# Optimization experiments

Hardware: AMD Instinct MI355X
Metric: run time of the kernel (lower is better)

Reference implementation:

```python
import jax, jax.numpy as jnp
import numpy as np

N_NODES = 50000
N_EDGES = 800000
IN_F, EDGE_F, HID, HEADS, OUT_F = 128, 16, 32, 4, 128
NEG_SLOPE = 0.2


def edge_gat_layer(h, ef, src, dst, W, We, al, ar, ae, b, act):
    """One DGL-style EdgeGATConv layer.
    h: [N, Fin], ef: [E, Fe], W: [Fin, H*D], We: [Fe, H*D],
    al/ar/ae: [H, D], b: [H*D]. Returns [N, H*D].
    """
    N = h.shape[0]
    H, D = al.shape
    feat = (h @ W).reshape(N, H, D)                    # [N,H,D]
    fe = (ef @ We).reshape(-1, H, D)                   # [E,H,D]
    el = jnp.einsum('nhd,hd->nh', feat, al)            # [N,H]
    er = jnp.einsum('nhd,hd->nh', feat, ar)            # [N,H]
    ee = jnp.einsum('ehd,hd->eh', fe, ae)              # [E,H]
    e = jax.nn.leaky_relu(el[src] + er[dst] + ee, NEG_SLOPE)  # [E,H]
    # edge softmax over incoming edges of each dst node
    emax = jax.ops.segment_max(e, dst, num_segments=N)        # [N,H]
    ex = jnp.exp(e - emax[dst])                               # [E,H]
    esum = jax.ops.segment_sum(ex, dst, num_segments=N)       # [N,H]
    a = ex / esum[dst]                                        # [E,H]
    msg = feat[src] * a[:, :, None]                           # [E,H,D]
    rst = jax.ops.segment_sum(msg, dst, num_segments=N)       # [N,H,D]
    rst = rst + b.reshape(1, H, D)
    if act:
        rst = jax.nn.relu(rst)
    return rst.reshape(N, H * D)


def _glorot(k, shape):
    fan = shape[0]
    return jax.random.normal(k, shape, dtype=jnp.float32) / np.sqrt(fan)


def setup_inputs() -> dict:
    key = jax.random.key(0)
    ks = jax.random.split(key, 24)
    inp = {
        'h': jax.random.normal(ks[0], (N_NODES, IN_F), dtype=jnp.float32),
        'edge_feats': jax.random.normal(ks[1], (N_EDGES, EDGE_F), dtype=jnp.float32),
        'src': jax.random.randint(ks[2], (N_EDGES,), 0, N_NODES, dtype=jnp.int32),
        'dst': jax.random.randint(ks[3], (N_EDGES,), 0, N_NODES, dtype=jnp.int32),
    }
    # layer 0: IN_F -> HEADS*HID ; layer 1: HEADS*HID -> HEADS*HID ; layer 2: heads=1, OUT_F
    dims = [(IN_F, HEADS, HID), (HEADS * HID, HEADS, HID), (HEADS * HID, 1, OUT_F)]
    ki = 4
    for i, (fin, H, D) in enumerate(dims):
        inp[f'W{i}'] = _glorot(ks[ki], (fin, H * D)); ki += 1
        inp[f'We{i}'] = _glorot(ks[ki], (EDGE_F, H * D)); ki += 1
        inp[f'al{i}'] = _glorot(ks[ki], (H, D)); ki += 1
        inp[f'ar{i}'] = _glorot(ks[ki], (H, D)); ki += 1
        inp[f'ae{i}'] = _glorot(ks[ki], (H, D)); ki += 1
        inp[f'b{i}'] = jnp.zeros((H * D,), dtype=jnp.float32)
    return inp


def reference(h, edge_feats, src, dst,
              W0, We0, al0, ar0, ae0, b0,
              W1, We1, al1, ar1, ae1, b1,
              W2, We2, al2, ar2, ae2, b2):
    h = edge_gat_layer(h, edge_feats, src, dst, W0, We0, al0, ar0, ae0, b0, True)
    h = edge_gat_layer(h, edge_feats, src, dst, W1, We1, al1, ar1, ae1, b1, True)
    h = edge_gat_layer(h, edge_feats, src, dst, W2, We2, al2, ar2, ae2, b2, False)
    return h
```

## Files before the change

### kernel.cpp

```cpp
#include <hip/hip_runtime.h>
#include <hip/hip_fp16.h>
#include <cstdint>

#define NN 50000
#define NE 800000
static constexpr int HD = 128;
static constexpr int EF_DIM = 16;
static constexpr int SCAN_B = 256;
static constexpr int NPARTS = (NN + SCAN_B - 1) / SCAN_B;
static constexpr int EBLK = (NE + 255) / 256;
static constexpr int FG = (NN + 63) / 64;

typedef _Float16 f16x4 __attribute__((ext_vector_type(4)));
typedef float f32x4 __attribute__((ext_vector_type(4)));

struct RecP {
    int src;
    int e;
    f16x4 p0;
    f16x4 p1;
    _Float16 p2;
    _Float16 pad;
};
union Rec32 { RecP r; float4 v[2]; };


__global__ void k_zero(int* __restrict__ cnt) {
    int i = blockIdx.x * blockDim.x + threadIdx.x;
    if (i < NN) cnt[i] = 0;
}

__global__ __launch_bounds__(256) void k_prep2(const float* __restrict__ h,
        const int* __restrict__ dst,
        const float* __restrict__ We0, const float* __restrict__ ae0,
        const float* __restrict__ We1, const float* __restrict__ ae1,
        const float* __restrict__ We2, const float* __restrict__ ae2,
        const float* __restrict__ W0, const float* __restrict__ W1,
        const float* __restrict__ W2,
        int* __restrict__ cnt, int* __restrict__ pos_loc, float* __restrict__ M,
        _Float16* __restrict__ Wht, _Float16* __restrict__ Xh) {
    int b = blockIdx.x;
    const int t = threadIdx.x;
    if (b < EBLK) {
        int e = b * 256 + t;
        if (e < NE) pos_loc[e] = atomicAdd(&cnt[dst[e]], 1);
        return;
    }
    b -= EBLK;
    if (b < 3) {
        int l = b;
        const float* We = (l == 0) ? We0 : (l == 1) ? We1 : We2;
        const float* ae = (l == 0) ? ae0 : (l == 1) ? ae1 : ae2;
        int H = (l == 2) ? 1 : 4, D = (l == 2) ? 128 : 32;
        if (t < EF_DIM * H) {
            int f = t / H, hh = t % H;
            float s = 0.f;
            for (int d = 0; d < D; d++) s += We[f * HD + hh * D + d] * ae[hh * D + d];
            M[l * 64 + f * H + hh] = s;
        }
        return;
    }
    if (b < 195) {
        int i = (b - 3) * 256 + t;
        int l = i >> 14, rem = i & 16383;
        int n = rem >> 7, k = rem & 127;
        const float* W = (l == 0) ? W0 : (l == 1) ? W1 : W2;
        Wht[(size_t)l * 16384 + n * 128 + k] = (_Float16)W[k * 128 + n];
        return;
    }
    {
        int i = (b - 195) * 256 + t;
        if (i < NN * 32) {
            float4 v = ((const float4*)h)[i];
            f16x4 o = {(_Float16)v.x, (_Float16)v.y, (_Float16)v.z, (_Float16)v.w};
            ((f16x4*)Xh)[i] = o;
        }
    }
}

__global__ __launch_bounds__(SCAN_B) void k_part(const int* __restrict__ deg,
                                                 int* __restrict__ part) {
    __shared__ int s[SCAN_B];
    int t = threadIdx.x;
    int i = blockIdx.x * SCAN_B + t;
    s[t] = (i < NN) ? deg[i] : 0;
    __syncthreads();
    for (int off = SCAN_B / 2; off > 0; off >>= 1) {
        if (t < off) s[t] += s[t + off];
        __syncthreads();
    }
    if (t == 0) part[blockIdx.x] = s[0];
}

__global__ __launch_bounds__(SCAN_B) void k_scanpart(int* __restrict__ part) {
    __shared__ int s[SCAN_B];
    int t = threadIdx.x;
    int v = (t < NPARTS) ? part[t] : 0;
    s[t] = v;
    __syncthreads();
    for (int off = 1; off < SCAN_B; off <<= 1) {
        int u = (t >= off) ? s[t - off] : 0;
        __syncthreads();
        s[t] += u;
        __syncthreads();
    }
    if (t < NPARTS) part[t] = s[t] - v;
}

__global__ __launch_bounds__(SCAN_B) void k_rowptr(const int* __restrict__ deg,
                                                   const int* __restrict__ part,
                                                   int* __restrict__ row_ptr) {
    __shared__ int s[SCAN_B];
    int t = threadIdx.x;
    int i = blockIdx.x * SCAN_B + t;
    int v = (i < NN) ? deg[i] : 0;
    s[t] = v;
    __syncthreads();
    for (int off = 1; off < SCAN_B; off <<= 1) {
        int u = (t >= off) ? s[t - off] : 0;
        __syncthreads();
        s[t] += u;
        __syncthreads();
    }
    int excl = s[t] - v + part[blockIdx.x];
    if (i < NN) row_ptr[i] = excl;
    if (i == NN) row_ptr[NN] = NE;
}

__global__ __launch_bounds__(256) void k_place(const int* __restrict__ src,
                                               const int* __restrict__ dst,
                                               const int* __restrict__ pos_loc,
                                               const float* __restrict__ EFt,
                                               const float* __restrict__ M,
                                               const int* __restrict__ row_ptr,
                                               float4* __restrict__ rec) {
    __shared__ float sM[192];
    int t = threadIdx.x;
    if (t < 192) sM[t] = M[t];
    __syncthreads();
    int e = blockIdx.x * 256 + t;
    if (e >= NE) return;
    float ef[EF_DIM];
    const float4* efp = (const float4*)(EFt + (size_t)e * EF_DIM);
#pragma unroll
    for (int q = 0; q < 4; q++) {
        float4 v = efp[q];
        ef[4 * q] = v.x; ef[4 * q + 1] = v.y; ef[4 * q + 2] = v.z; ef[4 * q + 3] = v.w;
    }
    float o0[4] = {0.f, 0.f, 0.f, 0.f};
    float o1[4] = {0.f, 0.f, 0.f, 0.f};
    float o2 = 0.f;
#pragma unroll
    for (int f = 0; f < EF_DIM; f++) {
        float v = ef[f];
#pragma unroll
        for (int hh = 0; hh < 4; hh++) {
            o0[hh] += v * sM[f * 4 + hh];
            o1[hh] += v * sM[64 + f * 4 + hh];
        }
        o2 += v * sM[128 + f];
    }
    Rec32 u;
    u.r.src = src[e];
    u.r.e = e;
    u.r.p0 = f16x4{(_Float16)o0[0], (_Float16)o0[1], (_Float16)o0[2], (_Float16)o0[3]};
    u.r.p1 = f16x4{(_Float16)o1[0], (_Float16)o1[1], (_Float16)o1[2], (_Float16)o1[3]};
    u.r.p2 = (_Float16)o2;
    u.r.pad = (_Float16)0.f;
    int pos = row_ptr[dst[e]] + pos_loc[e];
    rec[(size_t)pos * 2] = u.v[0];
    rec[(size_t)pos * 2 + 1] = u.v[1];
}

__global__ __launch_bounds__(256) void k_segsort2(const int* __restrict__ row_ptr,
                                                  const float4* __restrict__ rec,
                                                  int* __restrict__ ssrc,
                                                  f16x4* __restrict__ ep0,
                                                  f16x4* __restrict__ ep1,
                                                  _Float16* __restrict__ ep2) {
    __shared__ Rec32 seg[4][128];
    const int wave = threadIdx.x >> 6;
    const int lane = threadIdx.x & 63;
    const int n = blockIdx.x * 4 + wave;
    const int start = row_ptr[n];
    const int len = row_ptr[n + 1] - start;
    const bool small = (len > 0 && len <= 128);
    if (small)
        for (int s = lane; s < len; s += 64) {
            seg[wave][s].v[0] = rec[(size_t)(start + s) * 2];
            seg[wave][s].v[1] = rec[(size_t)(start + s) * 2 + 1];
        }
    __syncthreads();
    if (small) {
        for (int s = lane; s < len; s += 64) {
            RecP me = seg[wave][s].r;
            int rank = 0;
            for (int j = 0; j < len; j++) {
                const RecP& o = seg[wave][j].r;
                rank += (o.src < me.src) || (o.src == me.src && o.e < me.e);
            }
            int w = start + rank;
            ssrc[w] = me.src;
            ep0[w] = me.p0;
            ep1[w] = me.p1;
            ep2[w] = me.p2;
        }
    } else if (len > 128) {
        for (int s = lane; s < len; s += 64) {
            Rec32 u;
            u.v[0] = rec[(size_t)(start + s) * 2];
            u.v[1] = rec[(size_t)(start + s) * 2 + 1];
            int w = start + s;
            ssrc[w] = u.r.src;
            ep0[w] = u.r.p0;
            ep1[w] = u.r.p1;
            ep2[w] = u.r.p2;
        }
    }
}

template <int H>
__global__ __launch_bounds__(256) void k_feat(const _Float16* __restrict__ Xh,
                                              const _Float16* __restrict__ Wht,
                                              const float* __restrict__ al,
                                              const float* __restrict__ ar,
                                              _Float16* __restrict__ Fh,
                                              float* __restrict__ el,
                                              float* __restrict__ er) {
    const int t = threadIdx.x;
    const int lane = t & 63;
    const int wv = t >> 6;
    const int l15 = lane & 15;
    const int kg = lane >> 4;
    const int nbase = blockIdx.x * 64;
    const int arow = nbase + wv * 16 + l15;
    const int rclamp = (arow < NN) ? arow : NN - 1;
    const int ksub = kg * 4;
    f16x4 a[8];
#pragma unroll
    for (int kb = 0; kb < 8; kb++)
        a[kb] = *(const f16x4*)(Xh + (size_t)rclamp * 128 + kb * 16 + ksub);

    const int r0 = nbase + wv * 16 + kg * 4;
    float slp[4][H], srp[4][H];
#pragma unroll
    for (int r = 0; r < 4; r++)
#pragma unroll
        for (int hh = 0; hh < H; hh++) { slp[r][hh] = 0.f; srp[r][hh] = 0.f; }

#pragma unroll
    for (int nt = 0; nt < 8; nt++) {
        f32x4 acc = {0.f, 0.f, 0.f, 0.f};
        const int nc = nt * 16 + l15;
        const _Float16* wp = Wht + (size_t)nc * 128;
#pragma unroll
        for (int kb = 0; kb < 8; kb++) {
            f16x4 bf = *(const f16x4*)(wp + kb * 16 + ksub);
            acc = __builtin_amdgcn_mfma_f32_16x16x16f16(a[kb], bf, acc, 0, 0, 0);
        }
        const float alv = al[nc], arv = ar[nc];
        const int hsel = (H == 4) ? (nt >> 1) : 0;
#pragma unroll
        for (int r = 0; r < 4; r++) {
            int ro = r0 + r;
            if (ro < NN) Fh[(size_t)ro * 128 + nc] = (_Float16)acc[r];
            slp[r][hsel] += acc[r] * alv;
            srp[r][hsel] += acc[r] * arv;
        }
    }

#pragma unroll
    for (int m = 1; m < 16; m <<= 1)
#pragma unroll
        for (int r = 0; r < 4; r++)
#pragma unroll
            for (int hh = 0; hh < H; hh++) {
                slp[r][hh] += __shfl_xor(slp[r][hh], m);
                srp[r][hh] += __shfl_xor(srp[r][hh], m);
            }

    if (H == 4) {
        int r = l15 >> 2, hh2 = l15 & 3;
        float sv = 0.f, ev = 0.f;
#pragma unroll
        for (int rr = 0; rr < 4; rr++)
#pragma unroll
            for (int hc = 0; hc < H; hc++)
                if (rr == r && hc == hh2) { sv = slp[rr][hc]; ev = srp[rr][hc]; }
        int ro = r0 + r;
        if (ro < NN) { el[ro * 4 + hh2] = sv; er[ro * 4 + hh2] = ev; }
    } else {
        if (l15 < 4) {
            float sv = 0.f, ev = 0.f;
#pragma unroll
            for (int rr = 0; rr < 4; rr++)
                if (rr == l15) { sv = slp[rr][0]; ev = srp[rr][0]; }
            int ro = r0 + l15;
            if (ro < NN) { el[ro] = sv; er[ro] = ev; }
        }
    }
}

template <int H, int D, int OUT16>
__global__ __launch_bounds__(256) void k_node(const int* __restrict__ row_ptr,
                                              const int* __restrict__ ssrc,
                                              const _Float16* __restrict__ ep,
                                              const float* __restrict__ el,
                                              const float* __restrict__ er,
                                              const __half2* __restrict__ Fh,
                                              const float* __restrict__ bias,
                                              float* __restrict__ Rf,
                                              _Float16* __restrict__ Rh,
                                              int act) {
    __shared__ float wlds[4][256];
    const int wave = threadIdx.x >> 6;
    const int lane = threadIdx.x & 63;
    const int n = blockIdx.x * 4 + wave;
    const int start = row_ptr[n];
    const int end = row_ptr[n + 1];
    const int len = end - start;
    const int slots = len * H;
    const int c = 2 * lane;
    const int hcol = c / D;
    float2 b2 = make_float2(bias[c], bias[c + 1]);
    float2 a = make_float2(0.f, 0.f);

    if (len > 0) {
        constexpr int hsh = (H == 4) ? 2 : 0;
        const int hh = lane & (H - 1);
        const float er_j = er[n * H + hh];
        const _Float16* epb = ep + (size_t)start * H;
        float pmax = -3.0e38f, psum = 0.f;

        if (slots <= 256) {
            float* wp = wlds[wave];
            for (int jj = lane; jj < slots; jj += 64) {
                int i = start + (jj >> hsh);
                float x = el[ssrc[i] * H + hh] + er_j + (float)epb[jj];
                x = (x > 0.f) ? x : 0.2f * x;
                wp[jj] = x;
                pmax = fmaxf(pmax, x);
            }
            for (int m = H; m < 64; m <<= 1) pmax = fmaxf(pmax, __shfl_xor(pmax, m));
            for (int jj = lane; jj < slots; jj += 64) {
                float ex = __expf(wp[jj] - pmax);
                wp[jj] = ex;
                psum += ex;
            }
            for (int m = H; m < 64; m <<= 1) psum += __shfl_xor(psum, m);
            const float inv = 1.f / __shfl(psum, hcol);
#pragma unroll 8
            for (int i = start; i < end; i++) {
                float w = wp[(i - start) * H + hcol];
                float2 f2 = __half22float2(Fh[(size_t)ssrc[i] * 64 + lane]);
                a.x += f2.x * w;
                a.y += f2.y * w;
            }
            a.x *= inv;
            a.y *= inv;
        } else {
            for (int jj = lane; jj < slots; jj += 64) {
                int i = start + (jj >> hsh);
                float x = el[ssrc[i] * H + hh] + er_j + (float)epb[jj];
                x = (x > 0.f) ? x : 0.2f * x;
                pmax = fmaxf(pmax, x);
            }
            for (int m = H; m < 64; m <<= 1) pmax = fmaxf(pmax, __shfl_xor(pmax, m));
            for (int jj = lane; jj < slots; jj += 64) {
                int i = start + (jj >> hsh);
                float x = el[ssrc[i] * H + hh] + er_j + (float)epb[jj];
                x = (x > 0.f) ? x : 0.2f * x;
                psum += __expf(x - pmax);
            }
            for (int m = H; m < 64; m <<= 1) psum += __shfl_xor(psum, m);
            const float inv = 1.f / __shfl(psum, hcol);
            const float pm_c = __shfl(pmax, hcol);
            const float er_c = er[n * H + hcol];
            for (int i = start; i < end; i++) {
                int sn = ssrc[i];
                float x = el[sn * H + hcol] + er_c + (float)epb[(i - start) * H + hcol];
                x = (x > 0.f) ? x : 0.2f * x;
                float w = __expf(x - pm_c);
                float2 f2 = __half22float2(Fh[(size_t)sn * 64 + lane]);
                a.x += f2.x * w;
                a.y += f2.y * w;
            }
            a.x *= inv;
            a.y *= inv;
        }
    }

    float2 v = make_float2(a.x + b2.x, a.y + b2.y);
    if (act) { v.x = fmaxf(v.x, 0.f); v.y = fmaxf(v.y, 0.f); }
    if (OUT16)
        ((__half2*)Rh)[(size_t)n * 64 + lane] = __floats2half2_rn(v.x, v.y);
    else
        ((float2*)Rf)[(size_t)n * 64 + lane] = v;
}


extern "C" void kernel_launch(void* const* d_in, const int* in_sizes, int n_in,
                              void* d_out, int out_size, void* d_ws, size_t ws_size,
                              hipStream_t stream) {
    const float* h   = (const float*)d_in[0];
    const float* eft = (const float*)d_in[1];
    const int* src   = (const int*)d_in[2];
    const int* dst   = (const int*)d_in[3];
    auto P = [&](int i) { return (const float*)d_in[i]; };

    float* ws = (float*)d_ws;
    float4* rec    = (float4*)ws;
    _Float16* Xh   = (_Float16*)(ws + 6400000);
    _Float16* Wht  = Xh + (size_t)NN * 128;
    _Float16* ep0s = Wht + 3 * 16384;
    _Float16* ep1s = ep0s + (size_t)NE * 4;
    _Float16* ep2s = ep1s + (size_t)NE * 4;
    int* ssrc      = (int*)(ep2s + NE);
    int* pos_loc   = ssrc + NE;
    float* M       = (float*)(pos_loc + NE);
    int* row_ptr   = (int*)(M + 192);
    int* cnt       = row_ptr + (NN + 1);
    int* part      = cnt + NN;
    _Float16* Fh   = (_Float16*)(part + NPARTS + 64);
    float* el      = (float*)(Fh + (size_t)NN * 128);
    float* er      = el + (size_t)NN * 4;
    float* out     = (float*)d_out;

    hipLaunchKernelGGL(k_zero, dim3(NPARTS), dim3(256), 0, stream, cnt);
    hipLaunchKernelGGL(k_prep2, dim3(EBLK + 195 + (NN * 32 + 255) / 256), dim3(256), 0,
                       stream, h, dst, P(5), P(8), P(11), P(14), P(17), P(20),
                       P(4), P(10), P(16), cnt, pos_loc, M, Wht, Xh);
    hipLaunchKernelGGL(k_part, dim3(NPARTS), dim3(SCAN_B), 0, stream, cnt, part);
    hipLaunchKernelGGL(k_scanpart, dim3(1), dim3(SCAN_B), 0, stream, part);
    hipLaunchKernelGGL(k_rowptr, dim3(NPARTS), dim3(SCAN_B), 0, stream,
                       cnt, part, row_ptr);
    hipLaunchKernelGGL(k_place, dim3(EBLK), dim3(256), 0, stream,
                       src, dst, pos_loc, eft, M, row_ptr, rec);
    hipLaunchKernelGGL((k_feat<4>), dim3(FG), dim3(256), 0, stream,
                       Xh, Wht, P(6), P(7), Fh, el, er);
    hipLaunchKernelGGL(k_segsort2, dim3(NN / 4), dim3(256), 0, stream,
                       row_ptr, rec, ssrc, (f16x4*)ep0s, (f16x4*)ep1s, ep2s);

    hipLaunchKernelGGL((k_node<4, 32, 1>), dim3(NN / 4), dim3(256), 0, stream,
                       row_ptr, ssrc, ep0s, el, er, (const __half2*)Fh, P(9),
                       nullptr, Xh, 1);
    hipLaunchKernelGGL((k_feat<4>), dim3(FG), dim3(256), 0, stream,
                       Xh, Wht + 16384, P(12), P(13), Fh, el, er);
    hipLaunchKernelGGL((k_node<4, 32, 1>), dim3(NN / 4), dim3(256), 0, stream,
                       row_ptr, ssrc, ep1s, el, er, (const __half2*)Fh, P(15),
                       nullptr, Xh, 1);
    hipLaunchKernelGGL((k_feat<1>), dim3(FG), dim3(256), 0, stream,
                       Xh, Wht + 32768, P(18), P(19), Fh, el, er);
    hipLaunchKernelGGL((k_node<1, 128, 0>), dim3(NN / 4), dim3(256), 0, stream,
                       row_ptr, ssrc, ep2s, el, er, (const __half2*)Fh, P(21),
                       out, nullptr, 0);
}
```

Measured before the change: 370.6 us.

## Replace three-kernel row-pointer scan with single-pass decoupled look-back scan

Merges the partial-sum, partition-scan and row-pointer kernels into one kernel that uses decoupled look-back over per-block flag/value state words, which k_zero now clears. The aim is to drop two kernel launches and the extra passes over the degree array. It also moves k_segsort2 ahead of the first k_feat and lowers the unroll factor in the node aggregation loop from 8 to 4. Look-back relies on earlier blocks being scheduled before later ones finish spinning, which is normally true but is not formally guaranteed.

```diff
diff --git a/kernel.cpp b/kernel.cpp
--- a/kernel.cpp
+++ b/kernel.cpp
@@ -25,9 +25,10 @@
 union Rec32 { RecP r; float4 v[2]; };
 
 
-__global__ void k_zero(int* __restrict__ cnt) {
+__global__ void k_zero(int* __restrict__ cnt, unsigned* __restrict__ state) {
     int i = blockIdx.x * blockDim.x + threadIdx.x;
     if (i < NN) cnt[i] = 0;
+    if (i < NPARTS) state[i] = 0;
 }
 
 __global__ __launch_bounds__(256) void k_prep2(const float* __restrict__ h,
@@ -78,24 +79,14 @@
     }
 }
 
-__global__ __launch_bounds__(SCAN_B) void k_part(const int* __restrict__ deg,
-                                                 int* __restrict__ part) {
+__global__ __launch_bounds__(SCAN_B) void k_scan_lb(const int* __restrict__ cnt,
+                                                    int* __restrict__ row_ptr,
+                                                    unsigned* __restrict__ state) {
     __shared__ int s[SCAN_B];
-    int t = threadIdx.x;
-    int i = blockIdx.x * SCAN_B + t;
-    s[t] = (i < NN) ? deg[i] : 0;
-    __syncthreads();
-    for (int off = SCAN_B / 2; off > 0; off >>= 1) {
-        if (t < off) s[t] += s[t + off];
-        __syncthreads();
-    }
-    if (t == 0) part[blockIdx.x] = s[0];
-}
-
-__global__ __launch_bounds__(SCAN_B) void k_scanpart(int* __restrict__ part) {
-    __shared__ int s[SCAN_B];
-    int t = threadIdx.x;
-    int v = (t < NPARTS) ? part[t] : 0;
+    __shared__ int s_excl;
+    const int b = blockIdx.x, t = threadIdx.x;
+    const int i = b * SCAN_B + t;
+    int v = (i < NN) ? cnt[i] : 0;
     s[t] = v;
     __syncthreads();
     for (int off = 1; off < SCAN_B; off <<= 1) {
@@ -104,26 +95,30 @@
         s[t] += u;
         __syncthreads();
     }
-    if (t < NPARTS) part[t] = s[t] - v;
-}
-
-__global__ __launch_bounds__(SCAN_B) void k_rowptr(const int* __restrict__ deg,
-                                                   const int* __restrict__ part,
-                                                   int* __restrict__ row_ptr) {
-    __shared__ int s[SCAN_B];
-    int t = threadIdx.x;
-    int i = blockIdx.x * SCAN_B + t;
-    int v = (i < NN) ? deg[i] : 0;
-    s[t] = v;
+    const int agg = s[SCAN_B - 1];
+    if (t == 0) {
+        if (b == 0) {
+            atomicExch(&state[0], (2u << 30) | (unsigned)agg);
+            s_excl = 0;
+        } else {
+            atomicExch(&state[b], (1u << 30) | (unsigned)agg);
+            int excl = 0;
+            int j = b - 1;
+            while (true) {
+                unsigned st = atomicAdd(&state[j], 0u);
+                unsigned flag = st >> 30;
+                if (flag == 0u) continue;
+                excl += (int)(st & 0x3FFFFFFFu);
+                if (flag == 2u) break;
+                j--;
+            }
+            atomicExch(&state[b], (2u << 30) | (unsigned)(excl + agg));
+            s_excl = excl;
+        }
+    }
     __syncthreads();
-    for (int off = 1; off < SCAN_B; off <<= 1) {
-        int u = (t >= off) ? s[t - off] : 0;
-        __syncthreads();
-        s[t] += u;
-        __syncthreads();
-    }
-    int excl = s[t] - v + part[blockIdx.x];
-    if (i < NN) row_ptr[i] = excl;
+    const int excl = s_excl;
+    if (i < NN) row_ptr[i] = excl + s[t] - v;
     if (i == NN) row_ptr[NN] = NE;
 }
 
@@ -349,7 +344,7 @@
             }
             for (int m = H; m < 64; m <<= 1) psum += __shfl_xor(psum, m);
             const float inv = 1.f / __shfl(psum, hcol);
-#pragma unroll 8
+#pragma unroll 4
             for (int i = start; i < end; i++) {
                 float w = wp[(i - start) * H + hcol];
                 float2 f2 = __half22float2(Fh[(size_t)ssrc[i] * 64 + lane]);
@@ -420,27 +415,25 @@
     float* M       = (float*)(pos_loc + NE);
     int* row_ptr   = (int*)(M + 192);
     int* cnt       = row_ptr + (NN + 1);
-    int* part      = cnt + NN;
-    _Float16* Fh   = (_Float16*)(part + NPARTS + 64);
+    unsigned* state = (unsigned*)(cnt + NN);
+    _Float16* Fh   = (_Float16*)(state + NPARTS + 64);
     float* el      = (float*)(Fh + (size_t)NN * 128);
     float* er      = el + (size_t)NN * 4;
     float* out     = (float*)d_out;
 
-    hipLaunchKernelGGL(k_zero, dim3(NPARTS), dim3(256), 0, stream, cnt);
+    hipLaunchKernelGGL(k_zero, dim3(NPARTS), dim3(256), 0, stream, cnt, state);
     hipLaunchKernelGGL(k_prep2, dim3(EBLK + 195 + (NN * 32 + 255) / 256), dim3(256), 0,
                        stream, h, dst, P(5), P(8), P(11), P(14), P(17), P(20),
                        P(4), P(10), P(16), cnt, pos_loc, M, Wht, Xh);
-    hipLaunchKernelGGL(k_part, dim3(NPARTS), dim3(SCAN_B), 0, stream, cnt, part);
-    hipLaunchKernelGGL(k_scanpart, dim3(1), dim3(SCAN_B), 0, stream, part);
-    hipLaunchKernelGGL(k_rowptr, dim3(NPARTS), dim3(SCAN_B), 0, stream,
-                       cnt, part, row_ptr);
+    hipLaunchKernelGGL(k_scan_lb, dim3(NPARTS), dim3(SCAN_B), 0, stream,
+                       cnt, row_ptr, state);
     hipLaunchKernelGGL(k_place, dim3(EBLK), dim3(256), 0, stream,
                        src, dst, pos_loc, eft, M, row_ptr, rec);
+    hipLaunchKernelGGL(k_segsort2, dim3(NN / 4), dim3(256), 0, stream,
+                       row_ptr, rec, ssrc, (f16x4*)ep0s, (f16x4*)ep1s, ep2s);
+
     hipLaunchKernelGGL((k_feat<4>), dim3(FG), dim3(256), 0, stream,
                        Xh, Wht, P(6), P(7), Fh, el, er);
-    hipLaunchKernelGGL(k_segsort2, dim3(NN / 4), dim3(256), 0, stream,
-                       row_ptr, rec, ssrc, (f16x4*)ep0s, (f16x4*)ep1s, ep2s);
-
     hipLaunchKernelGGL((k_node<4, 32, 1>), dim3(NN / 4), dim3(256), 0, stream,
                        row_ptr, ssrc, ep0s, el, er, (const __half2*)Fh, P(9),
                        nullptr, Xh, 1);
```

Result: slower. 383.6 us (+3.5%).
